# Kernel optimization log

Measured on AMD Instinct MI355X. Metric: run time of the kernel, lower is better.

Reference implementation:

```python
import jax, jax.numpy as jnp
import numpy as np
import math

B = 50        # graphs per batch
NPG = 2000    # nodes per graph
EPG = 12000   # edges per graph
F_IN = 256
NHID = 128
RATIO = 0.8


def setup_inputs() -> dict:
    key = jax.random.key(0)
    ks = jax.random.split(key, 12)
    N = B * NPG
    src_loc = jax.random.randint(ks[0], (B, EPG), 0, NPG)
    dst_loc = jax.random.randint(ks[1], (B, EPG), 0, NPG)
    off = (jnp.arange(B) * NPG)[:, None]
    edge_index = jnp.stack([(src_loc + off).reshape(-1), (dst_loc + off).reshape(-1)]).astype(jnp.int32)

    def lin(k, fi, fo):
        return (jax.random.normal(k, (fi, fo), jnp.float32) / np.sqrt(fi).astype(np.float32))

    return {
        "x": jax.random.normal(ks[2], (N, F_IN), jnp.float32),
        "W1": lin(ks[3], F_IN, NHID), "b1": jnp.zeros(NHID, jnp.float32),
        "Ws1": lin(ks[4], NHID, 1), "bs1": jnp.zeros(1, jnp.float32),
        "W2": lin(ks[5], NHID, NHID), "b2": jnp.zeros(NHID, jnp.float32),
        "Ws2": lin(ks[6], NHID, 1), "bs2": jnp.zeros(1, jnp.float32),
        "W3": lin(ks[7], NHID, NHID), "b3": jnp.zeros(NHID, jnp.float32),
        "Ws3": lin(ks[8], NHID, 1), "bs3": jnp.zeros(1, jnp.float32),
        "Wl": lin(ks[9], 2 * NHID, NHID), "bl": jnp.zeros(NHID, jnp.float32),
        "edge_index": edge_index,
    }


def gcn_conv(x, W, b, src, dst, w, N):
    # PyG GCNConv: D^{-1/2} (A + I) D^{-1/2} X W + b, deg from edge weights + self loop
    h = x @ W
    deg = jax.ops.segment_sum(w, dst, num_segments=N) + 1.0
    dis = jax.lax.rsqrt(deg)
    norm = w * dis[src] * dis[dst]                       # [E]
    agg = jax.ops.segment_sum(h[src] * norm[:, None], dst, num_segments=N)
    return agg + h / deg[:, None] + b                    # self-loop norm = 1/deg


def sag_pool(x, src, dst, w, Ws, bs, n_per_graph):
    N = x.shape[0]
    k = math.ceil(RATIO * n_per_graph)
    score = gcn_conv(x, Ws, bs, src, dst, w, N)[:, 0]    # [N]
    _, topi = jax.lax.top_k(score.reshape(B, n_per_graph), k)
    perm = (topi + (jnp.arange(B) * n_per_graph)[:, None]).reshape(-1)
    x_new = x[perm] * jnp.tanh(score[perm])[:, None]
    # filter_adj: keep edges whose endpoints survive, reindex; dropped edges -> weight 0
    mapping = jnp.full((N,), -1, jnp.int32).at[perm].set(jnp.arange(B * k, dtype=jnp.int32))
    ns, nd = mapping[src], mapping[dst]
    valid = (ns >= 0) & (nd >= 0) & (w > 0)
    return (x_new, jnp.where(valid, ns, 0), jnp.where(valid, nd, 0),
            jnp.where(valid, w, jnp.zeros((), x.dtype)), k)


def readout(x, n):
    # global max pool || global mean pool (equal-size graphs, nodes grouped per graph)
    xr = x.reshape(B, n, -1)
    return jnp.concatenate([xr.max(axis=1), xr.mean(axis=1)], axis=-1)


def reference(x, W1, b1, Ws1, bs1, W2, b2, Ws2, bs2, W3, b3, Ws3, bs3, Wl, bl, edge_index):
    src, dst = edge_index[0], edge_index[1]
    w = jnp.ones(src.shape[0], x.dtype)
    n = NPG
    x = jax.nn.relu(gcn_conv(x, W1, b1, src, dst, w, B * n))
    x, src, dst, w, n = sag_pool(x, src, dst, w, Ws1, bs1, n)
    x1 = readout(x, n)
    x = jax.nn.relu(gcn_conv(x, W2, b2, src, dst, w, B * n))
    x, src, dst, w, n = sag_pool(x, src, dst, w, Ws2, bs2, n)
    x2 = readout(x, n)
    x = jax.nn.relu(gcn_conv(x, W3, b3, src, dst, w, B * n))
    x, src, dst, w, n = sag_pool(x, src, dst, w, Ws3, bs3, n)
    x3 = readout(x, n)
    return jax.nn.relu((x1 + x2 + x3) @ Wl + bl)
```

## Files before the change

### kernel.cpp

```cpp
#include <hip/hip_runtime.h>
#include <math.h>

#define B_GRAPHS 50
#define NPG0     2000
#define EPG      12000
#define F_IN_C   256
#define NHID     128
#define N0       (B_GRAPHS * NPG0)
#define NE       (B_GRAPHS * EPG)
#define RSEG     32
#define GSLOTS   7
#define CPAD     136
#define KMAX     1600

typedef _Float16 f16x8 __attribute__((ext_vector_type(8)));
typedef float    f32x4 __attribute__((ext_vector_type(4)));

static inline int cdiv(int a, int b) { return (a + b - 1) / b; }

__global__ void k_fill_start(int* __restrict__ cnt, float* __restrict__ accum) {
    int i = blockIdx.x * 256 + threadIdx.x;
    if (i < N0) cnt[i] = 0;
    if (i < B_GRAPHS * 256) accum[i] = 0.f;
}

__global__ void k_init_cvt(const int* __restrict__ ei, int* __restrict__ esrc,
                           int* __restrict__ edst, float* __restrict__ ew,
                           int* __restrict__ cnt,
                           const float* __restrict__ W1, const float* __restrict__ W2,
                           const float* __restrict__ W3, _Float16* __restrict__ WT1,
                           _Float16* __restrict__ WT2, _Float16* __restrict__ WT3) {
    int t = blockIdx.x * 256 + threadIdx.x;
    if (t < NE) {
        int d = ei[NE + t];
        esrc[t] = ei[t]; edst[t] = d; ew[t] = 1.0f;
        atomicAdd(&cnt[d], 1);
    }
    if (t < 128 * 256) {
        int n = t >> 8, kk = t & 255;
        WT1[t] = (_Float16)W1[kk * 128 + n];
    } else if (t < 128 * 256 + 128 * 128) {
        int u = t - 32768; int n = u >> 7, kk = u & 127;
        WT2[u] = (_Float16)W2[kk * 128 + n];
    } else if (t < 128 * 256 + 2 * 128 * 128) {
        int u = t - 49152; int n = u >> 7, kk = u & 127;
        WT3[u] = (_Float16)W3[kk * 128 + n];
    }
}

template<int FP32IN, int F, int GATHER>
__global__ __launch_bounds__(256) void k_gemm_ws(const void* __restrict__ Xin,
                                                 const _Float16* __restrict__ WT,
                                                 const int* __restrict__ perm,
                                                 const float* __restrict__ gate,
                                                 _Float16* __restrict__ H, int N) {
    constexpr int KH  = (F > 128) ? 128 : F;
    constexpr int K8H = KH / 8;
    constexpr int SMEMSZ = (128 * KH > 64 * CPAD) ? 128 * KH : 64 * CPAD;
    __shared__ _Float16 smem[SMEMSZ];
    const int tid  = threadIdx.x;
    const int wave = tid >> 6, lane = tid & 63;
    const int quad = lane >> 4, l16 = lane & 15;
    const int m_blk = blockIdx.x * 64;

    f32x4 acc[8];
#pragma unroll
    for (int j = 0; j < 8; ++j) acc[j] = {0.f, 0.f, 0.f, 0.f};

    int row0 = m_blk + wave * 16 + l16;
    if (row0 > N - 1) row0 = N - 1;
    _Float16 g0 = (_Float16)1.0f;
    if (GATHER) {
        g0 = (_Float16)gate[row0];
        row0 = perm[row0];
    }
    const int sx = l16 & 7;
    constexpr int NKQ = F / 32;

    if (FP32IN) {
        constexpr int PD = (NKQ < 4) ? NKQ : 4;
        const float* base0 = (const float*)Xin + (size_t)row0 * F + quad * 8;
        float4 p0[PD][2];
#pragma unroll
        for (int i = 0; i < PD; ++i) {
            p0[i][0] = ((const float4*)(base0 + i * 32))[0];
            p0[i][1] = ((const float4*)(base0 + i * 32))[1];
        }
#pragma unroll
        for (int c = tid; c < 128 * K8H; c += 256) {
            int n = c / K8H, k8 = c - n * K8H;
            f16x8 v = *(const f16x8*)&WT[(size_t)(n * (F / 8) + k8) * 8];
            *(f16x8*)&smem[n * KH + ((k8 ^ (n & 7)) << 3)] = v;
        }
        __syncthreads();
#pragma unroll
        for (int kq = 0; kq < NKQ; ++kq) {
            if (KH < F && kq == NKQ / 2) {
                __syncthreads();
#pragma unroll
                for (int c = tid; c < 128 * K8H; c += 256) {
                    int n = c / K8H, k8 = c - n * K8H;
                    f16x8 v = *(const f16x8*)&WT[(size_t)(n * (F / 8) + K8H + k8) * 8];
                    *(f16x8*)&smem[n * KH + ((k8 ^ (n & 7)) << 3)] = v;
                }
                __syncthreads();
            }
            const int b = kq % PD;
            float4 f0 = p0[b][0], f1 = p0[b][1];
            if (kq + PD < NKQ) {
                p0[b][0] = ((const float4*)(base0 + (kq + PD) * 32))[0];
                p0[b][1] = ((const float4*)(base0 + (kq + PD) * 32))[1];
            }
            f16x8 af0 = (f16x8){(_Float16)f0.x,(_Float16)f0.y,(_Float16)f0.z,(_Float16)f0.w,
                                (_Float16)f1.x,(_Float16)f1.y,(_Float16)f1.z,(_Float16)f1.w};
            f16x8 bf[8];
#pragma unroll
            for (int j = 0; j < 8; ++j)
                bf[j] = *(const f16x8*)&smem[(j * 16 + l16) * KH + (((((kq & 3) << 2) + quad) ^ sx) << 3)];
#pragma unroll
            for (int j = 0; j < 8; ++j)
                acc[j] = __builtin_amdgcn_mfma_f32_16x16x32_f16(af0, bf[j], acc[j], 0, 0, 0);
        }
    } else {
#pragma unroll
        for (int c = tid; c < 128 * K8H; c += 256) {
            int n = c / K8H, k8 = c - n * K8H;
            f16x8 v = *(const f16x8*)&WT[(size_t)(n * K8H + k8) * 8];
            *(f16x8*)&smem[n * KH + ((k8 ^ (n & 7)) << 3)] = v;
        }
        const _Float16* base0 = (const _Float16*)Xin + (size_t)row0 * F + quad * 8;
        f16x8 q0[NKQ];
#pragma unroll
        for (int i = 0; i < NKQ; ++i)
            q0[i] = *(const f16x8*)(base0 + i * 32);
        __syncthreads();
#pragma unroll
        for (int kq = 0; kq < NKQ; ++kq) {
            f16x8 af0 = q0[kq];
            if (GATHER) af0 = af0 * g0;
            f16x8 bf[8];
#pragma unroll
            for (int j = 0; j < 8; ++j)
                bf[j] = *(const f16x8*)&smem[(j * 16 + l16) * KH + (((((kq & 3) << 2) + quad) ^ sx) << 3)];
#pragma unroll
            for (int j = 0; j < 8; ++j)
                acc[j] = __builtin_amdgcn_mfma_f32_16x16x32_f16(af0, bf[j], acc[j], 0, 0, 0);
        }
    }
    __syncthreads();

    _Float16* sC = smem;
    const int rw = wave * 16;
#pragma unroll
    for (int j = 0; j < 8; ++j)
#pragma unroll
        for (int g = 0; g < 4; ++g)
            sC[(rw + quad * 4 + g) * CPAD + j * 16 + l16] = (_Float16)acc[j][g];
    __syncthreads();
    {
        int rr = tid >> 2;
        int cc = (tid & 3) * 32;
        int gr = m_blk + rr;
        if (gr < N) {
            _Float16* Hr = H + (size_t)gr * 128 + cc;
            const _Float16* Sr = sC + rr * CPAD + cc;
#pragma unroll
            for (int c = 0; c < 4; ++c)
                *(f16x8*)&Hr[c * 8] = *(const f16x8*)&Sr[c * 8];
        }
    }
}

__global__ __launch_bounds__(1024) void k_scancsr(const int* __restrict__ cnt,
                                                  int* __restrict__ offs,
                                                  const int* __restrict__ esrc,
                                                  const int* __restrict__ edst,
                                                  const float* __restrict__ ew,
                                                  int* __restrict__ csr_src,
                                                  float* __restrict__ csr_norm,
                                                  int npg) {
    __shared__ int ch[1024];
    __shared__ int scnt[2048];
    __shared__ int scur[2048];
    int b = blockIdx.x, tid = threadIdx.x;
    int base = b * npg;
    int per = (npg + 1023) >> 10;
    int s0 = tid * per;
    int s1 = s0 + per; if (s1 > npg) s1 = npg; if (s0 > npg) s0 = npg;
    int s = 0;
    for (int i = s0; i < s1; ++i) { int c = cnt[base + i]; scnt[i] = c; s += c; }
    ch[tid] = s;
    __syncthreads();
    for (int d = 1; d < 1024; d <<= 1) {
        int t = ch[tid] + ((tid >= d) ? ch[tid - d] : 0);
        __syncthreads();
        ch[tid] = t;
        __syncthreads();
    }
    int run = b * EPG + ch[tid] - s;
    for (int i = s0; i < s1; ++i) {
        offs[base + i] = run; scur[i] = run;
        run += scnt[i];
    }
    __syncthreads();
    int e0 = b * EPG;
    for (int e = tid; e < EPG; e += 1024) {
        float w = ew[e0 + e];
        if (w > 0.f) {
            int sN = esrc[e0 + e], d = edst[e0 + e];
            int pos = atomicAdd(&scur[d - base], 1);
            csr_src[pos] = sN;
            csr_norm[pos] = rsqrtf((float)(scnt[sN - base] + 1)) *
                            rsqrtf((float)(scnt[d - base] + 1));
        }
    }
}

__global__ __launch_bounds__(256) void k_agg(const _Float16* __restrict__ H,
                                             const int* __restrict__ csr_src,
                                             const float* __restrict__ csr_norm,
                                             const int* __restrict__ offs,
                                             const int* __restrict__ cnt,
                                             const float* __restrict__ bias,
                                             const float* __restrict__ Ws,
                                             _Float16* __restrict__ X,
                                             float* __restrict__ hs,
                                             int bpg, int npg) {
    int bi = blockIdx.x;
    int x = bi & 7, s = bi >> 3;
    int gslot = s / bpg, blk = s - gslot * bpg;
    int g = x + 8 * gslot;
    if (g >= B_GRAPHS) return;
    int node = g * npg + blk * 4 + (threadIdx.x >> 6);
    int lane = threadIdx.x & 63;
    int quad = lane >> 4, l16 = lane & 15;

    int st = offs[node], c = cnt[node], en = st + c;
    float acc[8];
#pragma unroll
    for (int j = 0; j < 8; ++j) acc[j] = 0.f;

    if (c > 0) {
        for (int e0 = st; e0 < en; e0 += 8) {
            int eA = e0 + quad, eB = eA + 4;
            int ecA = eA < en ? eA : en - 1;
            int ecB = eB < en ? eB : en - 1;
            int uA = csr_src[ecA], uB = csr_src[ecB];
            float nA = (eA < en) ? csr_norm[ecA] : 0.f;
            float nB = (eB < en) ? csr_norm[ecB] : 0.f;
            f16x8 hA = *(const f16x8*)&H[(size_t)uA * NHID + l16 * 8];
            f16x8 hB = *(const f16x8*)&H[(size_t)uB * NHID + l16 * 8];
#pragma unroll
            for (int j = 0; j < 8; ++j) acc[j] = fmaf((float)hA[j], nA, acc[j]);
#pragma unroll
            for (int j = 0; j < 8; ++j) acc[j] = fmaf((float)hB[j], nB, acc[j]);
        }
    }
#pragma unroll
    for (int j = 0; j < 8; ++j) {
        acc[j] += __shfl_xor(acc[j], 16, 64);
        acc[j] += __shfl_xor(acc[j], 32, 64);
    }
    float invd = 1.f / (float)(c + 1);
    f16x8 hn = *(const f16x8*)&H[(size_t)node * NHID + l16 * 8];
    float4 b0 = *(const float4*)&bias[l16 * 8];
    float4 b1 = *(const float4*)&bias[l16 * 8 + 4];
    float4 w0 = *(const float4*)&Ws[l16 * 8];
    float4 w1 = *(const float4*)&Ws[l16 * 8 + 4];
    const float bb[8] = {b0.x, b0.y, b0.z, b0.w, b1.x, b1.y, b1.z, b1.w};
    const float ww[8] = {w0.x, w0.y, w0.z, w0.w, w1.x, w1.y, w1.z, w1.w};
    float sd = 0.f;
    f16x8 o;
#pragma unroll
    for (int j = 0; j < 8; ++j) {
        float v = fmaxf(acc[j] + (float)hn[j] * invd + bb[j], 0.f);
        o[j] = (_Float16)v;
        sd = fmaf(v, ww[j], sd);
    }
    if (quad == 0)
        *(f16x8*)&X[(size_t)node * NHID + l16 * 8] = o;
    sd += __shfl_xor(sd, 1, 64);
    sd += __shfl_xor(sd, 2, 64);
    sd += __shfl_xor(sd, 4, 64);
    sd += __shfl_xor(sd, 8, 64);
    if (lane == 0) hs[node] = sd;
}

template<int REMAP, int COMB>
__global__ __launch_bounds__(1024) void k_scoretopk(const float* __restrict__ hs,
                                                    int* __restrict__ csr_src,
                                                    float* __restrict__ csr_norm,
                                                    int* __restrict__ offs,
                                                    const int* __restrict__ cnt,
                                                    const float* __restrict__ bs,
                                                    int* __restrict__ perm,
                                                    float* __restrict__ gate,
                                                    int* __restrict__ esrc,
                                                    int* __restrict__ edst,
                                                    float* __restrict__ ew,
                                                    int* __restrict__ cntN,
                                                    const float* __restrict__ pmax,
                                                    const float* __restrict__ psum,
                                                    float* __restrict__ accum,
                                                    int npg, int k) {
    __shared__ float ss[2048];
    __shared__ int   si[2048];
    __shared__ float shs[2048];
    __shared__ int   shist[KMAX];
    int b = blockIdx.x, tid = threadIdx.x;
    int base = b * npg;

    if (COMB) {
        if (tid < 2 * NHID) {
            int f = tid & 127;
            bool isSum = tid >= NHID;
            float a2 = isSum ? 0.f : -__builtin_inff();
            for (int s = 0; s < RSEG; ++s) {
                float v = (isSum ? psum : pmax)[(size_t)(b * RSEG + s) * NHID + f];
                a2 = isSum ? (a2 + v) : fmaxf(a2, v);
            }
            if (isSum) accum[b * 256 + 128 + f] += a2 / (float)npg;
            else       accum[b * 256 + f]       += a2;
        }
    }

    float bs0 = bs[0];
    for (int i = tid; i < 2048; i += 1024)
        shs[i] = (i < npg) ? hs[base + i] : 0.f;
    __syncthreads();
    for (int i = tid; i < 2048; i += 1024) {
        if (i < npg) {
            int st = offs[base + i], c = cnt[base + i];
            float a = 0.f;
            for (int e = st; e < st + c; ++e)
                a = fmaf(shs[csr_src[e] - base], csr_norm[e], a);
            ss[i] = a + shs[i] / (float)(c + 1) + bs0;
        } else {
            ss[i] = -__builtin_inff();
        }
        si[i] = i;
    }
    __syncthreads();

    const int wbase = (tid >> 6) << 7;
    const int l = tid & 63;
    float vL = ss[wbase + l],      vH = ss[wbase + 64 + l];
    int   iL = si[wbase + l],      iH = si[wbase + 64 + l];

    auto reg_steps = [&](int size, int smax) {
        for (int s = smax; s > 0; s >>= 1) {
            if (s == 64) {
                bool fwd = (((wbase + l) & size) == 0);
                bool bba = (vH > vL) || (vH == vL && iH < iL);
                if (fwd ? bba : !bba) {
                    float tv = vL; vL = vH; vH = tv;
                    int ti = iL; iL = iH; iH = ti;
                }
            } else {
                bool iR = ((l & s) == 0);
                float pv = __shfl_xor(vL, s, 64);
                int   pi = __shfl_xor(iL, s, 64);
                float sa = iR ? vL : pv, sb = iR ? pv : vL;
                int   ia = iR ? iL : pi, ib = iR ? pi : iL;
                bool bba = (sb > sa) || (sb == sa && ib < ia);
                bool fwd = (((wbase + l) & size) == 0);
                if (fwd ? bba : !bba) { vL = pv; iL = pi; }
                pv = __shfl_xor(vH, s, 64);
                pi = __shfl_xor(iH, s, 64);
                sa = iR ? vH : pv; sb = iR ? pv : vH;
                ia = iR ? iH : pi; ib = iR ? pi : iH;
                bba = (sb > sa) || (sb == sa && ib < ia);
                bool fwd2 = (((wbase + 64 + l) & size) == 0);
                if (fwd2 ? bba : !bba) { vH = pv; iH = pi; }
            }
        }
    };

    for (int size = 2; size <= 128; size <<= 1)
        reg_steps(size, size >> 1);
    for (int size = 256; size <= 2048; size <<= 1) {
        ss[wbase + l] = vL;      si[wbase + l] = iL;
        ss[wbase + 64 + l] = vH; si[wbase + 64 + l] = iH;
        __syncthreads();
        for (int stride = size >> 1; stride >= 128; stride >>= 1) {
            int i = ((tid & ~(stride - 1)) << 1) | (tid & (stride - 1));
            int j = i | stride;
            float sa = ss[i], sb = ss[j];
            int   ia = si[i], ib = si[j];
            bool bba = (sb > sa) || (sb == sa && ib < ia);
            bool fwd = ((i & size) == 0);
            if (fwd ? bba : !bba) { ss[i] = sb; ss[j] = sa; si[i] = ib; si[j] = ia; }
            __syncthreads();
        }
        vL = ss[wbase + l];      iL = si[wbase + l];
        vH = ss[wbase + 64 + l]; iH = si[wbase + 64 + l];
        reg_steps(size, 64);
    }
    ss[wbase + l] = vL;      si[wbase + l] = iL;
    ss[wbase + 64 + l] = vH; si[wbase + 64 + l] = iH;
    __syncthreads();

    int* smap = (int*)shs;
    for (int j = tid; j < npg; j += 1024) {
        int ol = si[j];
        if (j < k) {
            int newg = b * k + j;
            perm[newg] = base + ol;
            smap[ol] = newg;
            gate[newg] = tanhf(ss[j]);
        } else {
            smap[ol] = -1;
        }
    }
    if (REMAP) {
        for (int j = tid; j < k; j += 1024) shist[j] = 0;
        __syncthreads();
        int e0 = b * EPG;
        for (int e = tid; e < EPG; e += 1024) {
            int idx = e0 + e;
            float w = ew[idx];
            bool valid = false;
            int ns = 0, nd = 0;
            if (w > 0.f) {
                ns = smap[esrc[idx] - base];
                nd = smap[edst[idx] - base];
                valid = (ns >= 0) && (nd >= 0);
            }
            esrc[idx] = valid ? ns : 0;
            edst[idx] = valid ? nd : 0;
            ew[idx]   = valid ? w : 0.f;
            if (valid) atomicAdd(&shist[nd - b * k], 1);
        }
        __syncthreads();
        int* sscan = (int*)ss;
        int* scur  = si;
        int per2 = (k + 1023) >> 10;
        int t0 = tid * per2, t1 = t0 + per2;
        if (t1 > k) t1 = k; if (t0 > k) t0 = k;
        int sloc = 0;
        for (int i = t0; i < t1; ++i) sloc += shist[i];
        sscan[tid] = sloc;
        __syncthreads();
        for (int d = 1; d < 1024; d <<= 1) {
            int t = sscan[tid] + ((tid >= d) ? sscan[tid - d] : 0);
            __syncthreads();
            sscan[tid] = t;
            __syncthreads();
        }
        int run = b * EPG + sscan[tid] - sloc;
        for (int i = t0; i < t1; ++i) {
            offs[b * k + i] = run; scur[i] = run;
            cntN[b * k + i] = shist[i];
            run += shist[i];
        }
        __syncthreads();
        for (int e = tid; e < EPG; e += 1024) {
            int idx = e0 + e;
            float w = ew[idx];
            if (w > 0.f) {
                int ns = esrc[idx], nd = edst[idx];
                int pos = atomicAdd(&scur[nd - b * k], 1);
                csr_src[pos] = ns;
                csr_norm[pos] = rsqrtf((float)(shist[ns - b * k] + 1)) *
                                rsqrtf((float)(shist[nd - b * k] + 1));
            }
        }
    }
}

__global__ __launch_bounds__(128) void k_pool_readout(const _Float16* __restrict__ X,
                                                      const float* __restrict__ gate,
                                                      const int* __restrict__ perm,
                                                      float* __restrict__ pmax,
                                                      float* __restrict__ psum, int k) {
    int s = blockIdx.x, b = blockIdx.y, f = threadIdx.x;
    int j0 = (k * s) / RSEG, j1 = (k * (s + 1)) / RSEG;
    float mx = -__builtin_inff(), sm = 0.f;
    for (int j = j0; j < j1; ++j) {
        int g = b * k + j;
        int old = perm[g];
        float v = (float)X[(size_t)old * NHID + f] * gate[g];
        mx = fmaxf(mx, v);
        sm += v;
    }
    pmax[(size_t)(b * RSEG + s) * NHID + f] = mx;
    psum[(size_t)(b * RSEG + s) * NHID + f] = sm;
}

__global__ __launch_bounds__(128) void k_comb_final(const float* __restrict__ pmax,
                                                    const float* __restrict__ psum,
                                                    const float* __restrict__ accum,
                                                    const float* __restrict__ Wl,
                                                    const float* __restrict__ bl,
                                                    float* __restrict__ out, int k) {
    __shared__ float a[256];
    int b = blockIdx.x, f = threadIdx.x;
    float mx = -__builtin_inff(), sm = 0.f;
#pragma unroll
    for (int s = 0; s < RSEG; ++s) {
        mx = fmaxf(mx, pmax[(size_t)(b * RSEG + s) * NHID + f]);
        sm += psum[(size_t)(b * RSEG + s) * NHID + f];
    }
    a[f]       = accum[b * 256 + f] + mx;
    a[128 + f] = accum[b * 256 + 128 + f] + sm / (float)k;
    __syncthreads();
    float s = bl[f];
    for (int i = 0; i < 256; ++i) s = fmaf(a[i], Wl[i * NHID + f], s);
    out[b * NHID + f] = fmaxf(s, 0.f);
}

extern "C" void kernel_launch(void* const* d_in, const int* in_sizes, int n_in,
                              void* d_out, int out_size, void* d_ws, size_t ws_size,
                              hipStream_t stream) {
    const float* x0 = (const float*)d_in[0];
    const float* Wm[3] = {(const float*)d_in[1], (const float*)d_in[5], (const float*)d_in[9]};
    const float* bm[3] = {(const float*)d_in[2], (const float*)d_in[6], (const float*)d_in[10]};
    const float* Wsc[3] = {(const float*)d_in[3], (const float*)d_in[7], (const float*)d_in[11]};
    const float* bsc[3] = {(const float*)d_in[4], (const float*)d_in[8], (const float*)d_in[12]};
    const float* Wl = (const float*)d_in[13];
    const float* bl = (const float*)d_in[14];
    const int*   ei = (const int*)d_in[15];
    float* out = (float*)d_out;

    _Float16* bufA = (_Float16*)d_ws;
    _Float16* bufB = bufA + (size_t)N0 * NHID;
    _Float16* WT1  = bufB + (size_t)N0 * NHID;
    _Float16* WT2  = WT1 + 128 * 256;
    _Float16* WT3  = WT2 + 128 * 128;
    float* hs     = (float*)(WT3 + 128 * 128);
    float* gate   = hs + N0;
    float* accum  = gate + N0;
    float* pmax   = accum + B_GRAPHS * 256;
    float* psum   = pmax + B_GRAPHS * RSEG * NHID;
    int*   cntA   = (int*)(psum + B_GRAPHS * RSEG * NHID);
    int*   cntB   = cntA + N0;
    int*   offs   = cntB + N0;
    int*   perm   = offs + N0;
    int*   esrc   = perm + N0;
    int*   edst   = esrc + NE;
    float* ew     = (float*)(edst + NE);
    int*   csr_src= (int*)(ew + NE);
    float* csr_norm = (float*)(csr_src + NE);

    _Float16* WTs[3] = {WT1, WT2, WT3};
    const int EG = cdiv(NE, 256);

    k_fill_start<<<cdiv(N0, 256), 256, 0, stream>>>(cntA, accum);
    k_init_cvt<<<EG, 256, 0, stream>>>(ei, esrc, edst, ew, cntA,
                                       Wm[0], Wm[1], Wm[2], WT1, WT2, WT3);

    int npg = NPG0;
    _Float16* Hbuf = bufA; _Float16* Xbuf = bufB;

    for (int layer = 0; layer < 3; ++layer) {
        int N = B_GRAPHS * npg;
        int k = (npg * 4) / 5;
        int bpg = npg >> 2;
        int* cnt  = (layer == 1) ? cntB : cntA;
        int* cntN = (layer == 1) ? cntA : cntB;

        if (layer == 0) {
            k_gemm_ws<1, 256, 0><<<cdiv(N, 64), 256, 0, stream>>>(x0, WTs[0], perm, gate, Hbuf, N);
            k_scancsr<<<B_GRAPHS, 1024, 0, stream>>>(cnt, offs, esrc, edst, ew,
                                                     csr_src, csr_norm, npg);
        } else {
            k_gemm_ws<0, 128, 1><<<cdiv(N, 64), 256, 0, stream>>>(Xbuf, WTs[layer], perm, gate, Hbuf, N);
        }
        k_agg<<<8 * GSLOTS * bpg, 256, 0, stream>>>(Hbuf, csr_src, csr_norm, offs, cnt,
                                                    bm[layer], Wsc[layer], Xbuf, hs, bpg, npg);
        if (layer == 0)
            k_scoretopk<1, 0><<<B_GRAPHS, 1024, 0, stream>>>(hs, csr_src, csr_norm, offs, cnt,
                                                             bsc[layer], perm, gate,
                                                             esrc, edst, ew, cntN,
                                                             pmax, psum, accum, npg, k);
        else if (layer == 1)
            k_scoretopk<1, 1><<<B_GRAPHS, 1024, 0, stream>>>(hs, csr_src, csr_norm, offs, cnt,
                                                             bsc[layer], perm, gate,
                                                             esrc, edst, ew, cntN,
                                                             pmax, psum, accum, npg, k);
        else
            k_scoretopk<0, 1><<<B_GRAPHS, 1024, 0, stream>>>(hs, csr_src, csr_norm, offs, cnt,
                                                             bsc[layer], perm, gate,
                                                             esrc, edst, ew, cntN,
                                                             pmax, psum, accum, npg, k);
        k_pool_readout<<<dim3(RSEG, B_GRAPHS), 128, 0, stream>>>(Xbuf, gate, perm, pmax, psum, k);
        if (layer == 2)
            k_comb_final<<<B_GRAPHS, 128, 0, stream>>>(pmax, psum, accum, Wl, bl, out, k);

        npg = k;
    }
}
```

Before: 543.4 us.

## Fuse pooled-readout partial max/sum into next layer's gathered GEMM

The per-layer readout kernel for layers 0 and 1 is removed. Its per-segment max and sum partials are now computed inside the next layer's gathered GEMM, from the gated fp16 rows the GEMM already loads, using wave shuffles and a shared-memory reduction. The score/top-k combine step now takes a segment count that matches 64-row GEMM blocks, which relies on the per-graph node counts being divisible by 64. This saves two launches and a second gather of the pooled features, at the cost of extra shuffle work and two more barriers in the GEMM.

```diff
diff --git a/kernel.cpp b/kernel.cpp
--- a/kernel.cpp
+++ b/kernel.cpp
@@ -48,12 +48,14 @@
     }
 }
 
-template<int FP32IN, int F, int GATHER>
+template<int FP32IN, int F, int GATHER, int POOL>
 __global__ __launch_bounds__(256) void k_gemm_ws(const void* __restrict__ Xin,
                                                  const _Float16* __restrict__ WT,
                                                  const int* __restrict__ perm,
                                                  const float* __restrict__ gate,
-                                                 _Float16* __restrict__ H, int N) {
+                                                 _Float16* __restrict__ H, int N,
+                                                 float* __restrict__ pmax,
+                                                 float* __restrict__ psum) {
     constexpr int KH  = (F > 128) ? 128 : F;
     constexpr int K8H = KH / 8;
     constexpr int SMEMSZ = (128 * KH > 64 * CPAD) ? 128 * KH : 64 * CPAD;
@@ -70,12 +72,16 @@
     int row0 = m_blk + wave * 16 + l16;
     if (row0 > N - 1) row0 = N - 1;
     _Float16 g0 = (_Float16)1.0f;
+    float g0f = 1.0f;
     if (GATHER) {
-        g0 = (_Float16)gate[row0];
+        g0f = gate[row0];
+        g0 = (_Float16)g0f;
         row0 = perm[row0];
     }
     const int sx = l16 & 7;
     constexpr int NKQ = F / 32;
+
+    f16x8 q0[NKQ];
 
     if (FP32IN) {
         constexpr int PD = (NKQ < 4) ? NKQ : 4;
@@ -129,7 +135,6 @@
             *(f16x8*)&smem[n * KH + ((k8 ^ (n & 7)) << 3)] = v;
         }
         const _Float16* base0 = (const _Float16*)Xin + (size_t)row0 * F + quad * 8;
-        f16x8 q0[NKQ];
 #pragma unroll
         for (int i = 0; i < NKQ; ++i)
             q0[i] = *(const f16x8*)(base0 + i * 32);
@@ -167,6 +172,40 @@
 #pragma unroll
             for (int c = 0; c < 4; ++c)
                 *(f16x8*)&Hr[c * 8] = *(const f16x8*)&Sr[c * 8];
+        }
+    }
+    if (POOL && GATHER && !FP32IN) {
+        __syncthreads();
+        float* smax = (float*)smem;
+        float* ssum = smax + 4 * 128;
+#pragma unroll
+        for (int kq = 0; kq < NKQ; ++kq) {
+#pragma unroll
+            for (int j = 0; j < 8; ++j) {
+                float v = (float)q0[kq][j] * g0f;
+                float mx = v, sm = v;
+#pragma unroll
+                for (int s2 = 1; s2 < 16; s2 <<= 1) {
+                    mx = fmaxf(mx, __shfl_xor(mx, s2, 64));
+                    sm += __shfl_xor(sm, s2, 64);
+                }
+                if (l16 == 0) {
+                    int f = kq * 32 + quad * 8 + j;
+                    smax[wave * 128 + f] = mx;
+                    ssum[wave * 128 + f] = sm;
+                }
+            }
+        }
+        __syncthreads();
+        if (tid < 128) {
+            float mx = fmaxf(fmaxf(smax[tid], smax[128 + tid]),
+                             fmaxf(smax[256 + tid], smax[384 + tid]));
+            float sm = ssum[tid] + ssum[128 + tid] + ssum[256 + tid] + ssum[384 + tid];
+            int kprev = N / B_GRAPHS;
+            int g = m_blk / kprev;
+            int blkg = (m_blk - g * kprev) >> 6;
+            pmax[(size_t)(g * RSEG + blkg) * NHID + tid] = mx;
+            psum[(size_t)(g * RSEG + blkg) * NHID + tid] = sm;
         }
     }
 }
@@ -302,7 +341,7 @@
                                                     const float* __restrict__ pmax,
                                                     const float* __restrict__ psum,
                                                     float* __restrict__ accum,
-                                                    int npg, int k) {
+                                                    int npg, int k, int nseg) {
     __shared__ float ss[2048];
     __shared__ int   si[2048];
     __shared__ float shs[2048];
@@ -315,7 +354,7 @@
             int f = tid & 127;
             bool isSum = tid >= NHID;
             float a2 = isSum ? 0.f : -__builtin_inff();
-            for (int s = 0; s < RSEG; ++s) {
+            for (int s = 0; s < nseg; ++s) {
                 float v = (isSum ? psum : pmax)[(size_t)(b * RSEG + s) * NHID + f];
                 a2 = isSum ? (a2 + v) : fmaxf(a2, v);
             }
@@ -558,13 +597,16 @@
         int bpg = npg >> 2;
         int* cnt  = (layer == 1) ? cntB : cntA;
         int* cntN = (layer == 1) ? cntA : cntB;
+        int nseg = npg >> 6;
 
         if (layer == 0) {
-            k_gemm_ws<1, 256, 0><<<cdiv(N, 64), 256, 0, stream>>>(x0, WTs[0], perm, gate, Hbuf, N);
+            k_gemm_ws<1, 256, 0, 0><<<cdiv(N, 64), 256, 0, stream>>>(
+                x0, WTs[0], perm, gate, Hbuf, N, pmax, psum);
             k_scancsr<<<B_GRAPHS, 1024, 0, stream>>>(cnt, offs, esrc, edst, ew,
                                                      csr_src, csr_norm, npg);
         } else {
-            k_gemm_ws<0, 128, 1><<<cdiv(N, 64), 256, 0, stream>>>(Xbuf, WTs[layer], perm, gate, Hbuf, N);
+            k_gemm_ws<0, 128, 1, 1><<<cdiv(N, 64), 256, 0, stream>>>(
+                Xbuf, WTs[layer], perm, gate, Hbuf, N, pmax, psum);
         }
         k_agg<<<8 * GSLOTS * bpg, 256, 0, stream>>>(Hbuf, csr_src, csr_norm, offs, cnt,
                                                     bm[layer], Wsc[layer], Xbuf, hs, bpg, npg);
@@ -572,20 +614,22 @@
             k_scoretopk<1, 0><<<B_GRAPHS, 1024, 0, stream>>>(hs, csr_src, csr_norm, offs, cnt,
                                                              bsc[layer], perm, gate,
                                                              esrc, edst, ew, cntN,
-                                                             pmax, psum, accum, npg, k);
+                                                             pmax, psum, accum, npg, k, 0);
         else if (layer == 1)
             k_scoretopk<1, 1><<<B_GRAPHS, 1024, 0, stream>>>(hs, csr_src, csr_norm, offs, cnt,
                                                              bsc[layer], perm, gate,
                                                              esrc, edst, ew, cntN,
-                                                             pmax, psum, accum, npg, k);
+                                                             pmax, psum, accum, npg, k, nseg);
         else
             k_scoretopk<0, 1><<<B_GRAPHS, 1024, 0, stream>>>(hs, csr_src, csr_norm, offs, cnt,
                                                              bsc[layer], perm, gate,
                                                              esrc, edst, ew, cntN,
-                                                             pmax, psum, accum, npg, k);
-        k_pool_readout<<<dim3(RSEG, B_GRAPHS), 128, 0, stream>>>(Xbuf, gate, perm, pmax, psum, k);
-        if (layer == 2)
+                                                             pmax, psum, accum, npg, k, nseg);
+        if (layer == 2) {
+            k_pool_readout<<<dim3(RSEG, B_GRAPHS), 128, 0, stream>>>(Xbuf, gate, perm,
+                                                                     pmax, psum, k);
             k_comb_final<<<B_GRAPHS, 128, 0, stream>>>(pmax, psum, accum, Wl, bl, out, k);
+        }
 
         npg = k;
     }
```

New measurement: 539.2 us. About the same (-0.8%).
